# Optimization experiments

Measured on AMD Instinct MI355X. Metric: run time of the kernel, lower is better.

The kernel has to match this reference:

```python
import jax, jax.numpy as jnp
import numpy as np

N, E, HDIM, EDIM, MSG_H, UPD_H = 50000, 640000, 128, 32, 128, 128
LN_EPS = 1e-5


def setup_inputs() -> dict:
    key = jax.random.key(0)
    ks = jax.random.split(key, 12)
    def lin(k, fan_in, fan_out):
        return jax.random.normal(k, (fan_in, fan_out), dtype=jnp.float32) / np.sqrt(fan_in)
    h = jax.random.normal(ks[0], (N, HDIM), dtype=jnp.float32)
    edge_index = jax.random.randint(ks[1], (2, E), 0, N, dtype=jnp.int32)
    edge_attr = jax.random.normal(ks[2], (E, EDIM), dtype=jnp.float32)
    return {
        "h": h,
        "edge_index": edge_index,
        "edge_attr": edge_attr,
        # edge MLP: Linear(2*hdim+edim -> msg_hidden), ReLU, Linear(msg_hidden -> hdim)
        "ew1": lin(ks[3], 2 * HDIM + EDIM, MSG_H),
        "eb1": jnp.zeros((MSG_H,), jnp.float32),
        "ew2": lin(ks[4], MSG_H, HDIM),
        "eb2": jnp.zeros((HDIM,), jnp.float32),
        # node MLP: Linear(2*hdim -> upd_hidden), ReLU, Linear(upd_hidden -> hdim)
        "nw1": lin(ks[5], 2 * HDIM, UPD_H),
        "nb1": jnp.zeros((UPD_H,), jnp.float32),
        "nw2": lin(ks[6], UPD_H, HDIM),
        "nb2": jnp.zeros((HDIM,), jnp.float32),
        # LayerNorm(hdim)
        "gamma": jnp.ones((HDIM,), jnp.float32),
        "beta": jnp.zeros((HDIM,), jnp.float32),
    }


def reference(h, edge_index, edge_attr, ew1, eb1, ew2, eb2, nw1, nb1, nw2, nb2, gamma, beta):
    src, dst = edge_index[0], edge_index[1]
    # gather + concat -> edge MLP  (eval mode: dropout inactive, edge_dropout off)
    m_in = jnp.concatenate([h[src], h[dst], edge_attr], axis=1)       # [E, 2H+EDIM]
    m = jax.nn.relu(m_in @ ew1 + eb1) @ ew2 + eb2                     # [E, H]
    # scatter-add messages into destination nodes
    agg = jax.ops.segment_sum(m, dst, num_segments=h.shape[0])        # [N, H]
    # node update MLP
    u_in = jnp.concatenate([h, agg], axis=1)                          # [N, 2H]
    h_upd = jax.nn.relu(u_in @ nw1 + nb1) @ nw2 + nb2                 # [N, H]
    # residual + LayerNorm
    x = h + h_upd
    mu = jnp.mean(x, axis=-1, keepdims=True)
    var = jnp.mean(jnp.square(x - mu), axis=-1, keepdims=True)
    return (x - mu) * jax.lax.rsqrt(var + LN_EPS) * gamma + beta
```

## Files before the change

kernel.cpp:

```cpp
#include <hip/hip_runtime.h>
#include <cstdint>

#define HD 128
#define ED 32
#define BME 64
#define BMN 128
#define PAD_N 264
#define PAD_T 136
#define EGRID 512

typedef _Float16 f16;
typedef __attribute__((ext_vector_type(2))) _Float16 f16x2;
typedef __attribute__((ext_vector_type(4))) _Float16 f16x4;
typedef __attribute__((ext_vector_type(8))) _Float16 f16x8;
typedef __attribute__((ext_vector_type(4))) float    f32x4;
typedef __attribute__((ext_vector_type(4))) unsigned int u32x4;

__device__ __forceinline__ f32x4 mfma16(f16x8 a, f16x8 b, f32x4 c) {
    return __builtin_amdgcn_mfma_f32_16x16x32_f16(a, b, c, 0, 0, 0);
}
__device__ __forceinline__ f16x8 cvt8(const float* p) {
    const float4 a0 = *(const float4*)p;
    const float4 a1 = *(const float4*)(p + 4);
    f16x8 v;
    v[0] = (f16)a0.x; v[1] = (f16)a0.y; v[2] = (f16)a0.z; v[3] = (f16)a0.w;
    v[4] = (f16)a1.x; v[5] = (f16)a1.y; v[6] = (f16)a1.z; v[7] = (f16)a1.w;
    return v;
}
__device__ __forceinline__ void barrier_lds() {
    asm volatile("s_waitcnt lgkmcnt(0)" ::: "memory");
    __builtin_amdgcn_s_barrier();
    __builtin_amdgcn_sched_barrier(0);
}

__global__ __launch_bounds__(256) void zero_f32(float4* p, long n4) {
    long i = (long)blockIdx.x * blockDim.x + threadIdx.x;
    const long stride = (long)gridDim.x * blockDim.x;
    const float4 z = make_float4(0.f, 0.f, 0.f, 0.f);
    for (; i < n4; i += stride) p[i] = z;
}
__global__ __launch_bounds__(256) void zero_i32(int* p, int n) {
    int i = blockIdx.x * blockDim.x + threadIdx.x;
    if (i < n) p[i] = 0;
}
__global__ __launch_bounds__(256)
void cvt_f16_kernel(const float* __restrict__ x, f16* __restrict__ y, long n8) {
    long i = blockIdx.x * 256 + threadIdx.x;
    const long stride = (long)gridDim.x * 256;
    for (; i < n8; i += stride) *(f16x8*)(y + i * 8) = cvt8(x + i * 8);
}
__global__ __launch_bounds__(256)
void pack_all_kernel(const float* __restrict__ ew1, const float* __restrict__ ew2,
                     const float* __restrict__ nw1, const float* __restrict__ nw2,
                     f16* __restrict__ w1p, f16* __restrict__ w2p,
                     f16* __restrict__ n1p, f16* __restrict__ n2p)
{
    const int b = blockIdx.x;
    const float* w; f16* wp; int base;
    if (b < 18)      { w = ew1; wp = w1p; base = b; }
    else if (b < 26) { w = ew2; wp = w2p; base = b - 18; }
    else if (b < 42) { w = nw1; wp = n1p; base = b - 26; }
    else             { w = nw2; wp = n2p; base = b - 42; }
    const int idx = base * 256 + threadIdx.x;
    const int l  = idx & 63;
    const int fr = idx >> 6;
    const int wi = fr & 7, kt = fr >> 3;
    const int lii = l & 15, qq = l >> 4;
    const float* p = w + (size_t)(32 * kt + 8 * qq) * HD + 16 * wi + lii;
    f16x8 v;
#pragma unroll
    for (int e2 = 0; e2 < 8; ++e2) v[e2] = (f16)p[(size_t)e2 * HD];
    *(f16x8*)(wp + (size_t)idx * 8) = v;
}

__global__ __launch_bounds__(256)
void hist_kernel(const int* __restrict__ eidx, int* __restrict__ rank,
                 int* __restrict__ cnt, int E) {
    int e = blockIdx.x * 256 + threadIdx.x;
    if (e < E) rank[e] = atomicAdd(&cnt[eidx[E + e]], 1);
}
__global__ __launch_bounds__(1024)
void scan_kernel(const int* __restrict__ cnt, int* __restrict__ rs, int N) {
    __shared__ int wsum[16];
    __shared__ int s_carry;
    const int t = threadIdx.x, lane = t & 63, wid = t >> 6;
    if (t == 0) s_carry = 0;
    __syncthreads();
    for (int base = 0; base < N; base += 1024) {
        const int i = base + t;
        const int v = (i < N) ? cnt[i] : 0;
        int incl = v;
#pragma unroll
        for (int off = 1; off < 64; off <<= 1) {
            int u = __shfl_up(incl, off, 64);
            if (lane >= off) incl += u;
        }
        if (lane == 63) wsum[wid] = incl;
        __syncthreads();
        if (t == 0) {
            int s = 0;
#pragma unroll
            for (int w = 0; w < 16; ++w) { int x = wsum[w]; wsum[w] = s; s += x; }
        }
        __syncthreads();
        const int carry = s_carry;
        if (i < N) rs[i] = carry + wsum[wid] + incl - v;
        __syncthreads();
        if (t == 1023) s_carry = carry + wsum[15] + incl;
        __syncthreads();
    }
    if (threadIdx.x == 0) rs[N] = s_carry;
}
__global__ __launch_bounds__(256)
void pos_kernel(const int* __restrict__ eidx, const int* __restrict__ rs,
                int* __restrict__ pos, int E) {
    int e = blockIdx.x * 256 + threadIdx.x;
    if (e < E) pos[e] = rs[eidx[E + e]] + pos[e];
}

template <int MODE>
__global__ __launch_bounds__(512, 4)
void edge_kernel(const f16*   __restrict__ h16,
                 const int*   __restrict__ eidx,
                 const float* __restrict__ ea,
                 const f16*   __restrict__ w1p,
                 const float* __restrict__ b1,
                 const f16*   __restrict__ w2p,
                 const float* __restrict__ b2,
                 void*        __restrict__ aggm,
                 const int*   __restrict__ pos,
                 int E, int ntiles)
{
    __shared__ __align__(16) f16 sA[BME * 320];
    __shared__ __align__(16) f16 sT[BME * 128];
    __shared__ int sIdx[2][BME];

    const int t  = threadIdx.x;
    const int l  = t & 63;
    const int wv = t >> 6;
    const int li = l & 15;
    const int q  = l >> 4;
    const int lm = l & 7;
    const int r  = t >> 3;
    const int q8 = t & 7;

    f16x8 A1[9], A2[4];
#pragma unroll
    for (int kt = 0; kt < 9; ++kt)
        A1[kt] = *(const f16x8*)(w1p + ((size_t)(kt * 8 + wv) * 64 + l) * 8);
#pragma unroll
    for (int kt = 0; kt < 4; ++kt)
        A2[kt] = *(const f16x8*)(w2p + ((size_t)(kt * 8 + wv) * 64 + l) * 8);

    f16x8 d[4];
    f16x8 d4;
    int   psr = 0;
    auto prefetch = [&](int tile) {
        const int ec  = min(tile * BME + r, E - 1);
        const int src = eidx[ec];
        const int dst = eidx[E + ec];
        psr = (MODE == 0) ? dst : pos[ec];
        const f16* hs = h16 + (size_t)src * HD;
        const f16* hd = h16 + (size_t)dst * HD;
#pragma unroll
        for (int i = 0; i < 4; ++i) {
            const int c = (q8 + 8 * i) * 8;
            d[i] = (c < HD) ? *(const f16x8*)(hs + c)
                            : *(const f16x8*)(hd + (c - HD));
        }
        if (q8 < 4) d4 = cvt8(ea + (size_t)ec * ED + q8 * 8);
    };

    int tb = blockIdx.x;
    if (tb < ntiles) prefetch(tb);
    int par = 0;

    for (; tb < ntiles; tb += gridDim.x, par ^= 1) {
#pragma unroll
        for (int kt = 0; kt < 9; ++kt) asm volatile("" : "+v"(A1[kt]));
#pragma unroll
        for (int kt = 0; kt < 4; ++kt) asm volatile("" : "+v"(A2[kt]));

        {
            f16* row = sA + r * 320;
            const int sw = r & 7;
#pragma unroll
            for (int i = 0; i < 4; ++i) {
                const int ch = q8 + 8 * i;
                *(f16x8*)(row + ((ch ^ sw) * 8)) = d[i];
            }
            if (q8 < 4)
                *(f16x8*)(row + (((q8 + 32) ^ sw) * 8)) = d4;
            if (q8 == 0) sIdx[par][r] = psr;
        }
        barrier_lds();

        const int nt = tb + (int)gridDim.x;
        if (nt < ntiles) prefetch(nt);

        f32x4 acc[4];
#pragma unroll
        for (int j = 0; j < 4; ++j) acc[j] = (f32x4){0.f, 0.f, 0.f, 0.f};
#pragma unroll
        for (int kt = 0; kt < 9; ++kt) {
#pragma unroll
            for (int et = 0; et < 4; ++et) {
                const f16x8 b = *(const f16x8*)(sA + (16 * et + li) * 320
                                                + (((4 * kt + q) ^ lm) * 8));
                acc[et] = mfma16(A1[kt], b, acc[et]);
            }
        }

        {
            const int hidb = 16 * wv + 4 * q;
            const float4 bb = *(const float4*)(b1 + hidb);
            const int chT = hidb >> 3;
            const int off = hidb & 7;
#pragma unroll
            for (int et = 0; et < 4; ++et) {
                const f32x4 v = acc[et];
                float x0 = fmaxf(v[0] + bb.x, 0.f), x1 = fmaxf(v[1] + bb.y, 0.f);
                float x2 = fmaxf(v[2] + bb.z, 0.f), x3 = fmaxf(v[3] + bb.w, 0.f);
                f16x4 o; o[0] = (f16)x0; o[1] = (f16)x1; o[2] = (f16)x2; o[3] = (f16)x3;
                *(f16x4*)(sT + (16 * et + li) * 128 + ((chT ^ lm) * 8) + off) = o;
            }
        }
        barrier_lds();

        f32x4 acc2[4];
#pragma unroll
        for (int j = 0; j < 4; ++j) acc2[j] = (f32x4){0.f, 0.f, 0.f, 0.f};
#pragma unroll
        for (int kt = 0; kt < 4; ++kt) {
#pragma unroll
            for (int et = 0; et < 4; ++et) {
                const f16x8 b = *(const f16x8*)(sT + (16 * et + li) * 128
                                                + (((4 * kt + q) ^ lm) * 8));
                acc2[et] = mfma16(A2[kt], b, acc2[et]);
            }
        }

        if (MODE == 0) {
            float* agg = (float*)aggm;
            const int hidb = 16 * wv + 4 * q;
            const float4 bb = *(const float4*)(b2 + hidb);
#pragma unroll
            for (int et = 0; et < 4; ++et) {
                const int edge = 16 * et + li;
                if (tb * BME + edge < E) {
                    float* p = agg + (size_t)sIdx[par][edge] * HD + hidb;
                    const f32x4 v = acc2[et];
                    atomicAdd(p + 0, v[0] + bb.x);
                    atomicAdd(p + 1, v[1] + bb.y);
                    atomicAdd(p + 2, v[2] + bb.z);
                    atomicAdd(p + 3, v[3] + bb.w);
                }
            }
            barrier_lds();
        } else {
            barrier_lds();
            {
                const int hidb = 16 * wv + 4 * q;
                const float4 bb = *(const float4*)(b2 + hidb);
                const int chT = hidb >> 3;
                const int off = hidb & 7;
#pragma unroll
                for (int et = 0; et < 4; ++et) {
                    const f32x4 v = acc2[et];
                    f16x4 o;
                    o[0] = (f16)(v[0] + bb.x); o[1] = (f16)(v[1] + bb.y);
                    o[2] = (f16)(v[2] + bb.z); o[3] = (f16)(v[3] + bb.w);
                    *(f16x4*)(sT + (16 * et + li) * 128 + ((chT ^ lm) * 8) + off) = o;
                }
            }
            barrier_lds();
            f16* m = (f16*)aggm;
#pragma unroll
            for (int i = 0; i < 2; ++i) {
                const int idx  = t + i * 512;
                const int row2 = idx >> 4;
                const int c    = idx & 15;
                if (tb * BME + row2 < E) {
                    const f16x8 v = *(const f16x8*)(sT + row2 * 128
                                                    + ((c ^ (row2 & 7)) * 8));
                    __builtin_nontemporal_store(*(const u32x4*)&v,
                        (u32x4*)(m + (size_t)sIdx[par][row2] * HD + c * 8));
                }
            }
        }
    }
}

template <int CSR>
__global__ __launch_bounds__(256, 2)
void node_kernel(const f16*   __restrict__ h16,
                 const float* __restrict__ h,
                 const f16*   __restrict__ m,
                 const int*   __restrict__ rs,
                 const float* __restrict__ aggf,
                 const f16*   __restrict__ w1p,
                 const float* __restrict__ b1,
                 const f16*   __restrict__ w2p,
                 const float* __restrict__ b2,
                 const float* __restrict__ gamma,
                 const float* __restrict__ beta,
                 float*       __restrict__ out,
                 int N)
{
    __shared__ __align__(16) f16 sA[BMN * PAD_N];
    __shared__ float sMV[2 * BMN];

    const int t  = threadIdx.x;
    const int l  = t & 63;
    const int wv = t >> 6;
    const int li = l & 15;
    const int q  = l >> 4;
    const int nbase = blockIdx.x * BMN;

    {
        const int r = t >> 1, half = t & 1;
        const int node = min(nbase + r, N - 1);
        f16* rowp = sA + r * PAD_N;
        {
            const f16* srcp = h16 + (size_t)node * HD + half * 64;
#pragma unroll
            for (int i = 0; i < 8; ++i)
                *(f16x8*)(rowp + half * 64 + i * 8) = *(const f16x8*)(srcp + i * 8);
        }
        if (CSR) {
            const int s = rs[node], en = rs[node + 1];
            float ag[64];
#pragma unroll
            for (int i = 0; i < 64; ++i) ag[i] = 0.f;
            const f16* base = m + (size_t)s * HD + half * 64;
            for (int j = 0; j < en - s; ++j) {
                const f16* rp = base + (size_t)j * HD;
#pragma unroll
                for (int i = 0; i < 8; ++i) {
                    const f16x8 v = *(const f16x8*)(rp + i * 8);
#pragma unroll
                    for (int k2 = 0; k2 < 8; ++k2) ag[i * 8 + k2] += (float)v[k2];
                }
            }
#pragma unroll
            for (int i = 0; i < 8; ++i) {
                f16x8 o;
#pragma unroll
                for (int k2 = 0; k2 < 8; ++k2) o[k2] = (f16)ag[i * 8 + k2];
                *(f16x8*)(rowp + 128 + half * 64 + i * 8) = o;
            }
        } else {
            const float* srcp = aggf + (size_t)node * HD + half * 64;
#pragma unroll
            for (int i = 0; i < 8; ++i)
                *(f16x8*)(rowp + 128 + half * 64 + i * 8) = cvt8(srcp + i * 8);
        }
    }
    __syncthreads();

    f16x8 A1[2][8];
#pragma unroll
    for (int ht = 0; ht < 2; ++ht)
#pragma unroll
        for (int kt = 0; kt < 8; ++kt)
            A1[ht][kt] = *(const f16x8*)(w1p + ((size_t)(kt * 8 + wv * 2 + ht) * 64 + l) * 8);

    f32x4 acc[2][8];
#pragma unroll
    for (int i = 0; i < 2; ++i)
#pragma unroll
        for (int j = 0; j < 8; ++j) acc[i][j] = (f32x4){0.f, 0.f, 0.f, 0.f};
#pragma unroll
    for (int kt = 0; kt < 8; ++kt) {
#pragma unroll
        for (int et = 0; et < 8; ++et) {
            const f16x8 b = *(const f16x8*)(sA + (16 * et + li) * PAD_N + 32 * kt + 8 * q);
            acc[0][et] = mfma16(A1[0][kt], b, acc[0][et]);
            acc[1][et] = mfma16(A1[1][kt], b, acc[1][et]);
        }
    }
    __syncthreads();

    f16x8 A2[2][4];
#pragma unroll
    for (int ht = 0; ht < 2; ++ht)
#pragma unroll
        for (int kt = 0; kt < 4; ++kt)
            A2[ht][kt] = *(const f16x8*)(w2p + ((size_t)(kt * 8 + wv * 2 + ht) * 64 + l) * 8);

    f16* sT = sA;
#pragma unroll
    for (int ht = 0; ht < 2; ++ht) {
        const int hidb = 32 * wv + 16 * ht + 4 * q;
        const float4 bb = *(const float4*)(b1 + hidb);
#pragma unroll
        for (int et = 0; et < 8; ++et) {
            const f32x4 v = acc[ht][et];
            float x0 = fmaxf(v[0] + bb.x, 0.f), x1 = fmaxf(v[1] + bb.y, 0.f);
            float x2 = fmaxf(v[2] + bb.z, 0.f), x3 = fmaxf(v[3] + bb.w, 0.f);
            f16x4 o; o[0] = (f16)x0; o[1] = (f16)x1; o[2] = (f16)x2; o[3] = (f16)x3;
            *(f16x4*)(sT + (16 * et + li) * PAD_T + hidb) = o;
        }
    }
    __syncthreads();

    f32x4 acc2[2][8];
#pragma unroll
    for (int i = 0; i < 2; ++i)
#pragma unroll
        for (int j = 0; j < 8; ++j) acc2[i][j] = (f32x4){0.f, 0.f, 0.f, 0.f};
#pragma unroll
    for (int kt = 0; kt < 4; ++kt) {
#pragma unroll
        for (int et = 0; et < 8; ++et) {
            const f16x8 b = *(const f16x8*)(sT + (16 * et + li) * PAD_T + 32 * kt + 8 * q);
            acc2[0][et] = mfma16(A2[0][kt], b, acc2[0][et]);
            acc2[1][et] = mfma16(A2[1][kt], b, acc2[1][et]);
        }
    }
    __syncthreads();

    float* sX = (float*)sA;
#pragma unroll
    for (int ht = 0; ht < 2; ++ht) {
        const int hidb = 32 * wv + 16 * ht + 4 * q;
        const float4 bb = *(const float4*)(b2 + hidb);
#pragma unroll
        for (int et = 0; et < 8; ++et) {
            const int node = 16 * et + li;
            const int nc   = min(nbase + node, N - 1);
            const float4 hv = *(const float4*)(h + (size_t)nc * HD + hidb);
            const f32x4 v = acc2[ht][et];
            f32x4 x;
            x[0] = v[0] + bb.x + hv.x;
            x[1] = v[1] + bb.y + hv.y;
            x[2] = v[2] + bb.z + hv.z;
            x[3] = v[3] + bb.w + hv.w;
            *(f32x4*)(sX + (size_t)node * 132 + hidb) = x;
        }
    }
    __syncthreads();

    {
        const int node  = t >> 1;
        const int half2 = t & 1;
        const float* px = sX + node * 132 + half2 * 64;
        float s = 0.f, sq = 0.f;
#pragma unroll
        for (int i = 0; i < 16; ++i) {
            const float4 v = *(const float4*)(px + i * 4);
            s  += v.x + v.y + v.z + v.w;
            sq += v.x * v.x + v.y * v.y + v.z * v.z + v.w * v.w;
        }
        s  += __shfl_xor(s, 1);
        sq += __shfl_xor(sq, 1);
        if (!half2) {
            const float mean = s * (1.f / HD);
            const float var  = sq * (1.f / HD) - mean * mean;
            sMV[node]       = mean;
            sMV[BMN + node] = rsqrtf(var + 1e-5f);
        }
    }
    __syncthreads();

#pragma unroll
    for (int i = 0; i < 16; ++i) {
        const int idx  = t + i * 256;
        const int node = idx >> 5;
        const int c4   = (idx & 31) * 4;
        if (nbase + node < N) {
            const float4 xv = *(const float4*)(sX + node * 132 + c4);
            const float4 g4 = *(const float4*)(gamma + c4);
            const float4 b4 = *(const float4*)(beta + c4);
            const float mean = sMV[node];
            const float rstd = sMV[BMN + node];
            float4 o;
            o.x = (xv.x - mean) * rstd * g4.x + b4.x;
            o.y = (xv.y - mean) * rstd * g4.y + b4.y;
            o.z = (xv.z - mean) * rstd * g4.z + b4.z;
            o.w = (xv.w - mean) * rstd * g4.w + b4.w;
            *(float4*)(out + (size_t)(nbase + node) * HD + c4) = o;
        }
    }
}

extern "C" void kernel_launch(void* const* d_in, const int* in_sizes, int n_in,
                              void* d_out, int out_size, void* d_ws, size_t ws_size,
                              hipStream_t stream)
{
    const float* h     = (const float*)d_in[0];
    const int*   eidx  = (const int*)  d_in[1];
    const float* ea    = (const float*)d_in[2];
    const float* ew1   = (const float*)d_in[3];
    const float* eb1   = (const float*)d_in[4];
    const float* ew2   = (const float*)d_in[5];
    const float* eb2   = (const float*)d_in[6];
    const float* nw1   = (const float*)d_in[7];
    const float* nb1   = (const float*)d_in[8];
    const float* nw2   = (const float*)d_in[9];
    const float* nb2   = (const float*)d_in[10];
    const float* gamma = (const float*)d_in[11];
    const float* beta  = (const float*)d_in[12];
    float* out = (float*)d_out;

    const int N = in_sizes[0] / HD;
    const int E = in_sizes[1] / 2;
    const int ntiles = (E + BME - 1) / BME;

    size_t off = 0;
    auto alloc = [&](size_t bytes) {
        size_t o = off; off += (bytes + 255) & ~(size_t)255; return o;
    };
    const size_t o_m    = alloc((size_t)E * HD * sizeof(f16));
    const size_t o_h16  = alloc((size_t)N * HD * sizeof(f16));
    const size_t o_pos  = alloc((size_t)E * sizeof(int));
    const size_t o_rs   = alloc((size_t)(N + 1) * sizeof(int));
    const size_t o_cnt  = alloc((size_t)N * sizeof(int));
    const size_t o_w1p  = alloc((size_t)9 * 8 * 64 * 8 * sizeof(f16));
    const size_t o_w2p  = alloc((size_t)4 * 8 * 64 * 8 * sizeof(f16));
    const size_t o_n1p  = alloc((size_t)8 * 8 * 64 * 8 * sizeof(f16));
    const size_t o_n2p  = alloc((size_t)4 * 8 * 64 * 8 * sizeof(f16));
    const bool csr = (off <= ws_size);
    char* ws = (char*)d_ws;

    if (csr) {
        f16* mb   = (f16*)(ws + o_m);
        f16* h16  = (f16*)(ws + o_h16);
        int* pos  = (int*)(ws + o_pos);
        int* rs   = (int*)(ws + o_rs);
        int* cnt  = (int*)(ws + o_cnt);
        f16* w1p  = (f16*)(ws + o_w1p);
        f16* w2p  = (f16*)(ws + o_w2p);
        f16* n1p  = (f16*)(ws + o_n1p);
        f16* n2p  = (f16*)(ws + o_n2p);

        zero_i32<<<(N + 255) / 256, 256, 0, stream>>>(cnt, N);
        hist_kernel<<<(E + 255) / 256, 256, 0, stream>>>(eidx, pos, cnt, E);
        scan_kernel<<<1, 1024, 0, stream>>>(cnt, rs, N);
        pos_kernel<<<(E + 255) / 256, 256, 0, stream>>>(eidx, rs, pos, E);
        cvt_f16_kernel<<<2048, 256, 0, stream>>>(h, h16, (long)N * HD / 8);
        pack_all_kernel<<<50, 256, 0, stream>>>(ew1, ew2, nw1, nw2, w1p, w2p, n1p, n2p);
        edge_kernel<1><<<EGRID, 512, 0, stream>>>(
            h16, eidx, ea, w1p, eb1, w2p, eb2, (void*)mb, pos, E, ntiles);
        node_kernel<1><<<(N + BMN - 1) / BMN, 256, 0, stream>>>(
            h16, h, mb, rs, nullptr, n1p, nb1, n2p, nb2, gamma, beta, out, N);
    } else {
        size_t foff = 0;
        auto falloc = [&](size_t bytes) {
            size_t o = foff; foff += (bytes + 255) & ~(size_t)255; return o;
        };
        float* agg = (float*)(ws + falloc((size_t)N * HD * sizeof(float)));
        f16*   h16 = (f16*)  (ws + falloc((size_t)N * HD * sizeof(f16)));
        f16*   w1p = (f16*)  (ws + falloc((size_t)9 * 8 * 64 * 8 * sizeof(f16)));
        f16*   w2p = (f16*)  (ws + falloc((size_t)4 * 8 * 64 * 8 * sizeof(f16)));
        f16*   n1p = (f16*)  (ws + falloc((size_t)8 * 8 * 64 * 8 * sizeof(f16)));
        f16*   n2p = (f16*)  (ws + falloc((size_t)4 * 8 * 64 * 8 * sizeof(f16)));

        zero_f32<<<1024, 256, 0, stream>>>((float4*)agg, (long)N * HD / 4);
        cvt_f16_kernel<<<2048, 256, 0, stream>>>(h, h16, (long)N * HD / 8);
        pack_all_kernel<<<50, 256, 0, stream>>>(ew1, ew2, nw1, nw2, w1p, w2p, n1p, n2p);
        edge_kernel<0><<<EGRID, 512, 0, stream>>>(
            h16, eidx, ea, w1p, eb1, w2p, eb2, (void*)agg, nullptr, E, ntiles);
        node_kernel<0><<<(N + BMN - 1) / BMN, 256, 0, stream>>>(
            h16, h, nullptr, nullptr, agg, n1p, nb1, n2p, nb2, gamma, beta, out, N);
    }
}
```

Baseline: 285.6 us.

## Shrink edge tile to 32 edges with 256-thread blocks, two hidden tiles per wave

Edge tile size drops from 64 to 32 edges and the block from 512 to 256 threads (4 waves). Each wave now keeps two hidden-column slices of both weight matrices in registers, so every LDS B-fragment read feeds two MFMAs. The asm register pins are removed. Intent: better B-operand reuse and smaller per-block LDS/sync cost, traded against doubled weight registers per thread, lower launch-bound occupancy (2 blocks) and twice as many tile iterations with a fixed grid. The sA/sT shared arrays are still sized for BME, so they shrink accordingly.

```diff
diff --git a/kernel.cpp b/kernel.cpp
--- a/kernel.cpp
+++ b/kernel.cpp
@@ -3,7 +3,7 @@
 
 #define HD 128
 #define ED 32
-#define BME 64
+#define BME 32
 #define BMN 128
 #define PAD_N 264
 #define PAD_T 136
@@ -119,7 +119,7 @@
 }
 
 template <int MODE>
-__global__ __launch_bounds__(512, 4)
+__global__ __launch_bounds__(256, 2)
 void edge_kernel(const f16*   __restrict__ h16,
                  const int*   __restrict__ eidx,
                  const float* __restrict__ ea,
@@ -144,13 +144,16 @@
     const int r  = t >> 3;
     const int q8 = t & 7;
 
-    f16x8 A1[9], A2[4];
-#pragma unroll
-    for (int kt = 0; kt < 9; ++kt)
-        A1[kt] = *(const f16x8*)(w1p + ((size_t)(kt * 8 + wv) * 64 + l) * 8);
-#pragma unroll
-    for (int kt = 0; kt < 4; ++kt)
-        A2[kt] = *(const f16x8*)(w2p + ((size_t)(kt * 8 + wv) * 64 + l) * 8);
+    f16x8 A1[2][9], A2[2][4];
+#pragma unroll
+    for (int ht = 0; ht < 2; ++ht) {
+#pragma unroll
+        for (int kt = 0; kt < 9; ++kt)
+            A1[ht][kt] = *(const f16x8*)(w1p + ((size_t)(kt * 8 + wv * 2 + ht) * 64 + l) * 8);
+#pragma unroll
+        for (int kt = 0; kt < 4; ++kt)
+            A2[ht][kt] = *(const f16x8*)(w2p + ((size_t)(kt * 8 + wv * 2 + ht) * 64 + l) * 8);
+    }
 
     f16x8 d[4];
     f16x8 d4;
@@ -176,11 +179,6 @@
     int par = 0;
 
     for (; tb < ntiles; tb += gridDim.x, par ^= 1) {
-#pragma unroll
-        for (int kt = 0; kt < 9; ++kt) asm volatile("" : "+v"(A1[kt]));
-#pragma unroll
-        for (int kt = 0; kt < 4; ++kt) asm volatile("" : "+v"(A2[kt]));
-
         {
             f16* row = sA + r * 320;
             const int sw = r & 7;
@@ -198,86 +196,97 @@
         const int nt = tb + (int)gridDim.x;
         if (nt < ntiles) prefetch(nt);
 
-        f32x4 acc[4];
-#pragma unroll
-        for (int j = 0; j < 4; ++j) acc[j] = (f32x4){0.f, 0.f, 0.f, 0.f};
+        f32x4 acc[2][2];
+#pragma unroll
+        for (int i = 0; i < 2; ++i)
+#pragma unroll
+            for (int j = 0; j < 2; ++j) acc[i][j] = (f32x4){0.f, 0.f, 0.f, 0.f};
 #pragma unroll
         for (int kt = 0; kt < 9; ++kt) {
 #pragma unroll
-            for (int et = 0; et < 4; ++et) {
-                const f16x8 b = *(const f16x8*)(sA + (16 * et + li) * 320
+            for (int e = 0; e < 2; ++e) {
+                const f16x8 b = *(const f16x8*)(sA + (16 * e + li) * 320
                                                 + (((4 * kt + q) ^ lm) * 8));
-                acc[et] = mfma16(A1[kt], b, acc[et]);
-            }
-        }
-
-        {
-            const int hidb = 16 * wv + 4 * q;
+                acc[0][e] = mfma16(A1[0][kt], b, acc[0][e]);
+                acc[1][e] = mfma16(A1[1][kt], b, acc[1][e]);
+            }
+        }
+
+#pragma unroll
+        for (int ht = 0; ht < 2; ++ht) {
+            const int hidb = 32 * wv + 16 * ht + 4 * q;
             const float4 bb = *(const float4*)(b1 + hidb);
             const int chT = hidb >> 3;
             const int off = hidb & 7;
 #pragma unroll
-            for (int et = 0; et < 4; ++et) {
-                const f32x4 v = acc[et];
+            for (int e = 0; e < 2; ++e) {
+                const f32x4 v = acc[ht][e];
                 float x0 = fmaxf(v[0] + bb.x, 0.f), x1 = fmaxf(v[1] + bb.y, 0.f);
                 float x2 = fmaxf(v[2] + bb.z, 0.f), x3 = fmaxf(v[3] + bb.w, 0.f);
                 f16x4 o; o[0] = (f16)x0; o[1] = (f16)x1; o[2] = (f16)x2; o[3] = (f16)x3;
-                *(f16x4*)(sT + (16 * et + li) * 128 + ((chT ^ lm) * 8) + off) = o;
+                *(f16x4*)(sT + (16 * e + li) * 128 + ((chT ^ lm) * 8) + off) = o;
             }
         }
         barrier_lds();
 
-        f32x4 acc2[4];
-#pragma unroll
-        for (int j = 0; j < 4; ++j) acc2[j] = (f32x4){0.f, 0.f, 0.f, 0.f};
+        f32x4 acc2[2][2];
+#pragma unroll
+        for (int i = 0; i < 2; ++i)
+#pragma unroll
+            for (int j = 0; j < 2; ++j) acc2[i][j] = (f32x4){0.f, 0.f, 0.f, 0.f};
 #pragma unroll
         for (int kt = 0; kt < 4; ++kt) {
 #pragma unroll
-            for (int et = 0; et < 4; ++et) {
-                const f16x8 b = *(const f16x8*)(sT + (16 * et + li) * 128
+            for (int e = 0; e < 2; ++e) {
+                const f16x8 b = *(const f16x8*)(sT + (16 * e + li) * 128
                                                 + (((4 * kt + q) ^ lm) * 8));
-                acc2[et] = mfma16(A2[kt], b, acc2[et]);
+                acc2[0][e] = mfma16(A2[0][kt], b, acc2[0][e]);
+                acc2[1][e] = mfma16(A2[1][kt], b, acc2[1][e]);
             }
         }
 
         if (MODE == 0) {
             float* agg = (float*)aggm;
-            const int hidb = 16 * wv + 4 * q;
-            const float4 bb = *(const float4*)(b2 + hidb);
-#pragma unroll
-            for (int et = 0; et < 4; ++et) {
-                const int edge = 16 * et + li;
-                if (tb * BME + edge < E) {
-                    float* p = agg + (size_t)sIdx[par][edge] * HD + hidb;
-                    const f32x4 v = acc2[et];
-                    atomicAdd(p + 0, v[0] + bb.x);
-                    atomicAdd(p + 1, v[1] + bb.y);
-                    atomicAdd(p + 2, v[2] + bb.z);
-                    atomicAdd(p + 3, v[3] + bb.w);
+#pragma unroll
+            for (int ht = 0; ht < 2; ++ht) {
+                const int hidb = 32 * wv + 16 * ht + 4 * q;
+                const float4 bb = *(const float4*)(b2 + hidb);
+#pragma unroll
+                for (int e = 0; e < 2; ++e) {
+                    const int edge = 16 * e + li;
+                    if (tb * BME + edge < E) {
+                        float* p = agg + (size_t)sIdx[par][edge] * HD + hidb;
+                        const f32x4 v = acc2[ht][e];
+                        atomicAdd(p + 0, v[0] + bb.x);
+                        atomicAdd(p + 1, v[1] + bb.y);
+                        atomicAdd(p + 2, v[2] + bb.z);
+                        atomicAdd(p + 3, v[3] + bb.w);
+                    }
                 }
             }
             barrier_lds();
         } else {
             barrier_lds();
-            {
-                const int hidb = 16 * wv + 4 * q;
+#pragma unroll
+            for (int ht = 0; ht < 2; ++ht) {
+                const int hidb = 32 * wv + 16 * ht + 4 * q;
                 const float4 bb = *(const float4*)(b2 + hidb);
                 const int chT = hidb >> 3;
                 const int off = hidb & 7;
 #pragma unroll
-                for (int et = 0; et < 4; ++et) {
-                    const f32x4 v = acc2[et];
+                for (int e = 0; e < 2; ++e) {
+                    const f32x4 v = acc2[ht][e];
                     f16x4 o;
                     o[0] = (f16)(v[0] + bb.x); o[1] = (f16)(v[1] + bb.y);
                     o[2] = (f16)(v[2] + bb.z); o[3] = (f16)(v[3] + bb.w);
-                    *(f16x4*)(sT + (16 * et + li) * 128 + ((chT ^ lm) * 8) + off) = o;
+                    *(f16x4*)(sT + (16 * e + li) * 128 + ((chT ^ lm) * 8) + off) = o;
                 }
             }
             barrier_lds();
             f16* m = (f16*)aggm;
 #pragma unroll
             for (int i = 0; i < 2; ++i) {
-                const int idx  = t + i * 512;
+                const int idx  = t + i * 256;
                 const int row2 = idx >> 4;
                 const int c    = idx & 15;
                 if (tb * BME + row2 < E) {
@@ -540,7 +549,7 @@
         pos_kernel<<<(E + 255) / 256, 256, 0, stream>>>(eidx, rs, pos, E);
         cvt_f16_kernel<<<2048, 256, 0, stream>>>(h, h16, (long)N * HD / 8);
         pack_all_kernel<<<50, 256, 0, stream>>>(ew1, ew2, nw1, nw2, w1p, w2p, n1p, n2p);
-        edge_kernel<1><<<EGRID, 512, 0, stream>>>(
+        edge_kernel<1><<<EGRID, 256, 0, stream>>>(
             h16, eidx, ea, w1p, eb1, w2p, eb2, (void*)mb, pos, E, ntiles);
         node_kernel<1><<<(N + BMN - 1) / BMN, 256, 0, stream>>>(
             h16, h, mb, rs, nullptr, n1p, nb1, n2p, nb2, gamma, beta, out, N);
@@ -559,7 +568,7 @@
         zero_f32<<<1024, 256, 0, stream>>>((float4*)agg, (long)N * HD / 4);
         cvt_f16_kernel<<<2048, 256, 0, stream>>>(h, h16, (long)N * HD / 8);
         pack_all_kernel<<<50, 256, 0, stream>>>(ew1, ew2, nw1, nw2, w1p, w2p, n1p, n2p);
-        edge_kernel<0><<<EGRID, 512, 0, stream>>>(
+        edge_kernel<0><<<EGRID, 256, 0, stream>>>(
             h16, eidx, ea, w1p, eb1, w2p, eb2, (void*)agg, nullptr, E, ntiles);
         node_kernel<0><<<(N + BMN - 1) / BMN, 256, 0, stream>>>(
             h16, h, nullptr, nullptr, agg, n1p, nb1, n2p, nb2, gamma, beta, out, N);
```

Measured after the change: 265.7 us (median of 2 runs). 7.0% less time.

## Retile edge MLP to 32-edge tiles with 4 hidden tiles per wave

Applied to the files above, without the earlier changes.

Edge tile size drops from 64 to 32 edges and the block from 512 to 256 threads. Each wave now owns one 16-edge group and four 16-wide hidden tiles, so one LDS B-fragment load is reused across four MFMAs instead of one A register being reused across four edge groups. The first-layer weights stay in registers (36 f16x8 per lane) and the second-layer weights are reloaded from global memory every tile. This trades higher register pressure and repeated weight fetches for fewer LDS reads per MFMA and smaller LDS use. It also lowers per-block parallelism at a fixed grid of 512 blocks.

```diff
diff --git a/kernel.cpp b/kernel.cpp
--- a/kernel.cpp
+++ b/kernel.cpp
@@ -3,7 +3,7 @@
 
 #define HD 128
 #define ED 32
-#define BME 64
+#define BME 32
 #define BMN 128
 #define PAD_N 264
 #define PAD_T 136
@@ -119,7 +119,7 @@
 }
 
 template <int MODE>
-__global__ __launch_bounds__(512, 4)
+__global__ __launch_bounds__(256, 2)
 void edge_kernel(const f16*   __restrict__ h16,
                  const int*   __restrict__ eidx,
                  const float* __restrict__ ea,
@@ -138,19 +138,20 @@
     const int t  = threadIdx.x;
     const int l  = t & 63;
     const int wv = t >> 6;
+    const int hw = wv & 1;
+    const int eg = wv >> 1;
     const int li = l & 15;
     const int q  = l >> 4;
     const int lm = l & 7;
     const int r  = t >> 3;
     const int q8 = t & 7;
 
-    f16x8 A1[9], A2[4];
-#pragma unroll
-    for (int kt = 0; kt < 9; ++kt)
-        A1[kt] = *(const f16x8*)(w1p + ((size_t)(kt * 8 + wv) * 64 + l) * 8);
-#pragma unroll
-    for (int kt = 0; kt < 4; ++kt)
-        A2[kt] = *(const f16x8*)(w2p + ((size_t)(kt * 8 + wv) * 64 + l) * 8);
+    f16x8 A1[4][9];
+#pragma unroll
+    for (int ht = 0; ht < 4; ++ht)
+#pragma unroll
+        for (int kt = 0; kt < 9; ++kt)
+            A1[ht][kt] = *(const f16x8*)(w1p + ((size_t)(kt * 8 + 4 * hw + ht) * 64 + l) * 8);
 
     f16x8 d[4];
     f16x8 d4;
@@ -176,11 +177,6 @@
     int par = 0;
 
     for (; tb < ntiles; tb += gridDim.x, par ^= 1) {
-#pragma unroll
-        for (int kt = 0; kt < 9; ++kt) asm volatile("" : "+v"(A1[kt]));
-#pragma unroll
-        for (int kt = 0; kt < 4; ++kt) asm volatile("" : "+v"(A2[kt]));
-
         {
             f16* row = sA + r * 320;
             const int sw = r & 7;
@@ -195,6 +191,13 @@
         }
         barrier_lds();
 
+        f16x8 A2[4][4];
+#pragma unroll
+        for (int ht = 0; ht < 4; ++ht)
+#pragma unroll
+            for (int kt = 0; kt < 4; ++kt)
+                A2[ht][kt] = *(const f16x8*)(w2p + ((size_t)(kt * 8 + 4 * hw + ht) * 64 + l) * 8);
+
         const int nt = tb + (int)gridDim.x;
         if (nt < ntiles) prefetch(nt);
 
@@ -203,27 +206,24 @@
         for (int j = 0; j < 4; ++j) acc[j] = (f32x4){0.f, 0.f, 0.f, 0.f};
 #pragma unroll
         for (int kt = 0; kt < 9; ++kt) {
-#pragma unroll
-            for (int et = 0; et < 4; ++et) {
-                const f16x8 b = *(const f16x8*)(sA + (16 * et + li) * 320
-                                                + (((4 * kt + q) ^ lm) * 8));
-                acc[et] = mfma16(A1[kt], b, acc[et]);
-            }
-        }
-
-        {
-            const int hidb = 16 * wv + 4 * q;
+            const f16x8 b = *(const f16x8*)(sA + (16 * eg + li) * 320
+                                            + (((4 * kt + q) ^ lm) * 8));
+#pragma unroll
+            for (int ht = 0; ht < 4; ++ht)
+                acc[ht] = mfma16(A1[ht][kt], b, acc[ht]);
+        }
+
+#pragma unroll
+        for (int ht = 0; ht < 4; ++ht) {
+            const int hidb = 64 * hw + 16 * ht + 4 * q;
             const float4 bb = *(const float4*)(b1 + hidb);
             const int chT = hidb >> 3;
             const int off = hidb & 7;
-#pragma unroll
-            for (int et = 0; et < 4; ++et) {
-                const f32x4 v = acc[et];
-                float x0 = fmaxf(v[0] + bb.x, 0.f), x1 = fmaxf(v[1] + bb.y, 0.f);
-                float x2 = fmaxf(v[2] + bb.z, 0.f), x3 = fmaxf(v[3] + bb.w, 0.f);
-                f16x4 o; o[0] = (f16)x0; o[1] = (f16)x1; o[2] = (f16)x2; o[3] = (f16)x3;
-                *(f16x4*)(sT + (16 * et + li) * 128 + ((chT ^ lm) * 8) + off) = o;
-            }
+            const f32x4 v = acc[ht];
+            float x0 = fmaxf(v[0] + bb.x, 0.f), x1 = fmaxf(v[1] + bb.y, 0.f);
+            float x2 = fmaxf(v[2] + bb.z, 0.f), x3 = fmaxf(v[3] + bb.w, 0.f);
+            f16x4 o; o[0] = (f16)x0; o[1] = (f16)x1; o[2] = (f16)x2; o[3] = (f16)x3;
+            *(f16x4*)(sT + (16 * eg + li) * 128 + ((chT ^ lm) * 8) + off) = o;
         }
         barrier_lds();
 
@@ -232,24 +232,23 @@
         for (int j = 0; j < 4; ++j) acc2[j] = (f32x4){0.f, 0.f, 0.f, 0.f};
 #pragma unroll
         for (int kt = 0; kt < 4; ++kt) {
-#pragma unroll
-            for (int et = 0; et < 4; ++et) {
-                const f16x8 b = *(const f16x8*)(sT + (16 * et + li) * 128
-                                                + (((4 * kt + q) ^ lm) * 8));
-                acc2[et] = mfma16(A2[kt], b, acc2[et]);
-            }
+            const f16x8 b = *(const f16x8*)(sT + (16 * eg + li) * 128
+                                            + (((4 * kt + q) ^ lm) * 8));
+#pragma unroll
+            for (int ht = 0; ht < 4; ++ht)
+                acc2[ht] = mfma16(A2[ht][kt], b, acc2[ht]);
         }
 
         if (MODE == 0) {
             float* agg = (float*)aggm;
-            const int hidb = 16 * wv + 4 * q;
-            const float4 bb = *(const float4*)(b2 + hidb);
-#pragma unroll
-            for (int et = 0; et < 4; ++et) {
-                const int edge = 16 * et + li;
+#pragma unroll
+            for (int ht = 0; ht < 4; ++ht) {
+                const int hidb = 64 * hw + 16 * ht + 4 * q;
+                const float4 bb = *(const float4*)(b2 + hidb);
+                const int edge = 16 * eg + li;
                 if (tb * BME + edge < E) {
                     float* p = agg + (size_t)sIdx[par][edge] * HD + hidb;
-                    const f32x4 v = acc2[et];
+                    const f32x4 v = acc2[ht];
                     atomicAdd(p + 0, v[0] + bb.x);
                     atomicAdd(p + 1, v[1] + bb.y);
                     atomicAdd(p + 2, v[2] + bb.z);
@@ -259,25 +258,23 @@
             barrier_lds();
         } else {
             barrier_lds();
-            {
-                const int hidb = 16 * wv + 4 * q;
+#pragma unroll
+            for (int ht = 0; ht < 4; ++ht) {
+                const int hidb = 64 * hw + 16 * ht + 4 * q;
                 const float4 bb = *(const float4*)(b2 + hidb);
                 const int chT = hidb >> 3;
                 const int off = hidb & 7;
-#pragma unroll
-                for (int et = 0; et < 4; ++et) {
-                    const f32x4 v = acc2[et];
-                    f16x4 o;
-                    o[0] = (f16)(v[0] + bb.x); o[1] = (f16)(v[1] + bb.y);
-                    o[2] = (f16)(v[2] + bb.z); o[3] = (f16)(v[3] + bb.w);
-                    *(f16x4*)(sT + (16 * et + li) * 128 + ((chT ^ lm) * 8) + off) = o;
-                }
+                const f32x4 v = acc2[ht];
+                f16x4 o;
+                o[0] = (f16)(v[0] + bb.x); o[1] = (f16)(v[1] + bb.y);
+                o[2] = (f16)(v[2] + bb.z); o[3] = (f16)(v[3] + bb.w);
+                *(f16x4*)(sT + (16 * eg + li) * 128 + ((chT ^ lm) * 8) + off) = o;
             }
             barrier_lds();
             f16* m = (f16*)aggm;
 #pragma unroll
             for (int i = 0; i < 2; ++i) {
-                const int idx  = t + i * 512;
+                const int idx  = t + i * 256;
                 const int row2 = idx >> 4;
                 const int c    = idx & 15;
                 if (tb * BME + row2 < E) {
@@ -540,7 +537,7 @@
         pos_kernel<<<(E + 255) / 256, 256, 0, stream>>>(eidx, rs, pos, E);
         cvt_f16_kernel<<<2048, 256, 0, stream>>>(h, h16, (long)N * HD / 8);
         pack_all_kernel<<<50, 256, 0, stream>>>(ew1, ew2, nw1, nw2, w1p, w2p, n1p, n2p);
-        edge_kernel<1><<<EGRID, 512, 0, stream>>>(
+        edge_kernel<1><<<EGRID, 256, 0, stream>>>(
             h16, eidx, ea, w1p, eb1, w2p, eb2, (void*)mb, pos, E, ntiles);
         node_kernel<1><<<(N + BMN - 1) / BMN, 256, 0, stream>>>(
             h16, h, mb, rs, nullptr, n1p, nb1, n2p, nb2, gamma, beta, out, N);
@@ -559,7 +556,7 @@
         zero_f32<<<1024, 256, 0, stream>>>((float4*)agg, (long)N * HD / 4);
         cvt_f16_kernel<<<2048, 256, 0, stream>>>(h, h16, (long)N * HD / 8);
         pack_all_kernel<<<50, 256, 0, stream>>>(ew1, ew2, nw1, nw2, w1p, w2p, n1p, n2p);
-        edge_kernel<0><<<EGRID, 512, 0, stream>>>(
+        edge_kernel<0><<<EGRID, 256, 0, stream>>>(
             h16, eidx, ea, w1p, eb1, w2p, eb2, (void*)agg, nullptr, E, ntiles);
         node_kernel<0><<<(N + BMN - 1) / BMN, 256, 0, stream>>>(
             h16, h, nullptr, nullptr, agg, n1p, nb1, n2p, nb2, gamma, beta, out, N);
```

Result: slower. 562.1 us (+96.8%).
